# Kernel tuning notes

Hardware: AMD Instinct MI355X
Metric: run time of the kernel (lower is better)

Reference implementation:

```python
import jax, jax.numpy as jnp
import numpy as np

# Fixed production-scale sizes (equal-sized graphs so unbatch == reshape)
B, NQ, ND = 64, 32, 512     # graph pairs, query nodes/graph, data nodes/graph
DIN, D, K = 64, 128, 16     # GCN_in_size, GCN_out_size, NTN_k
DEG = 8                     # average degree


def _gcn(x, src, dst, W, b):
    """GCNConv with self loops + symmetric normalization (PyG semantics)."""
    N = x.shape[0]
    loop = jnp.arange(N)
    s = jnp.concatenate([src, loop])
    t = jnp.concatenate([dst, loop])
    deg = jax.ops.segment_sum(jnp.ones_like(t, x.dtype), t, num_segments=N)
    dinv = jnp.where(deg > 0, deg ** -0.5, 0.0)
    norm = (dinv[s] * dinv[t])[:, None]
    h = x @ W
    return jax.ops.segment_sum(h[s] * norm, t, num_segments=N) + b


def _three_gcn(x, ei, W1, b1, W2, b2, W3, b3):
    src, dst = ei[0], ei[1]
    h1 = jax.nn.relu(_gcn(x, src, dst, W1, b1))
    h2 = jax.nn.relu(_gcn(h1, src, dst, W2, b2))
    h3 = jax.nn.relu(_gcn(h2, src, dst, W3, b3))
    return h1, h2, h3


def _level(q, d, Wn, Vn, bn, cw, cb):
    """att_layer + NTN + elementwise mult + 1x1 conv + softmax over data nodes.
    q: [B,NQ,D], d: [B,ND,D] -> (softmaxed map [B,NQ,ND], raw map, he [B,K,NQ,ND])."""
    att = jax.nn.softmax(jnp.einsum('bqd,bnd->bqn', q, d) / jnp.sqrt(jnp.float32(D)), axis=-1)
    qW = jnp.einsum('bqd,kde->bkqe', q, Wn)           # [B,K,NQ,D]
    bil = jnp.einsum('bkqe,bne->bkqn', qW, d)          # [B,K,NQ,ND]
    lq = jnp.einsum('kd,bqd->bkq', Vn[:, :D], q)[:, :, :, None]
    ld = jnp.einsum('kd,bnd->bkn', Vn[:, D:], d)[:, :, None, :]
    he = jax.nn.sigmoid(bil + lq + ld + bn[None, :, None, None]) * att[:, None]
    e_raw = jnp.einsum('k,bkqn->bqn', cw, he) + cb     # 1x1 Conv2d(K->1)
    return jax.nn.softmax(e_raw, axis=-1), e_raw, he


def reference(x_d, edge_index_d, x_q, edge_index_q, batch_index_d, batch_index_q,
              W1, b1, W2, b2, W3, b3,
              Wn1, Vn1, bn1, cw1, cb1,
              Wn2, Vn2, bn2, cw2, cb2,
              Wn3, Vn3, bn3, cw3, cb3,
              w_end, b_end):
    d1, d2, d3 = _three_gcn(x_d, edge_index_d, W1, b1, W2, b2, W3, b3)
    q1, q2, q3 = _three_gcn(x_q, edge_index_q, W1, b1, W2, b2, W3, b3)
    # unbatch: batch indices are sorted with equal graph sizes -> reshape
    d1, d2, d3 = (t.reshape(B, ND, D) for t in (d1, d2, d3))
    q1, q2, q3 = (t.reshape(B, NQ, D) for t in (q1, q2, q3))
    e1, _, he1 = _level(q1, d1, Wn1, Vn1, bn1, cw1, cb1)
    _, e2raw, he2 = _level(q2, d2, Wn2, Vn2, bn2, cw2, cb2)
    e3, _, he3 = _level(q3, d3, Wn3, Vn3, bn3, cw3, cb3)
    # Faithful to source quirks: the zip unpack `e1,e2,e3,h1,h2,h1` rebinds h1 to
    # he_3 (he_1 is never used, he_3 appears twice) and end2 enters the concat
    # PRE-softmax (the softmaxed version was assigned to unused `nd2`).
    stack = jnp.concatenate([e1[:, None], e2raw[:, None], e3[:, None], he3, he2, he3], axis=1)
    out = jnp.einsum('c,bcqn->bqn', w_end, stack) + b_end  # con_end 1x1 conv + squeeze
    return jax.nn.softmax(out, axis=-1)                    # softmax over data nodes


def setup_inputs() -> dict:
    key = jax.random.key(0)
    k = jax.random.split(key, 40)
    n = jax.random.normal
    Nd, Nq = B * ND, B * NQ
    Ed, Eq = Nd * DEG, Nq * DEG
    gid_d = jnp.repeat(jnp.arange(B), ND * DEG)
    gid_q = jnp.repeat(jnp.arange(B), NQ * DEG)
    inp = {
        'x_d': n(k[0], (Nd, DIN), jnp.float32),
        'x_q': n(k[1], (Nq, DIN), jnp.float32),
        'edge_index_d': jnp.stack([jax.random.randint(k[2], (Ed,), 0, ND) + gid_d * ND,
                                   jax.random.randint(k[3], (Ed,), 0, ND) + gid_d * ND]),
        'edge_index_q': jnp.stack([jax.random.randint(k[4], (Eq,), 0, NQ) + gid_q * NQ,
                                   jax.random.randint(k[5], (Eq,), 0, NQ) + gid_q * NQ]),
        'batch_index_d': jnp.repeat(jnp.arange(B), ND),
        'batch_index_q': jnp.repeat(jnp.arange(B), NQ),
        'W1': n(k[6], (DIN, D), jnp.float32) / np.sqrt(DIN), 'b1': jnp.zeros((D,), jnp.float32),
        'W2': n(k[7], (D, D), jnp.float32) / np.sqrt(D), 'b2': jnp.zeros((D,), jnp.float32),
        'W3': n(k[8], (D, D), jnp.float32) / np.sqrt(D), 'b3': jnp.zeros((D,), jnp.float32),
    }
    for i, l in enumerate(('1', '2', '3')):
        inp['Wn' + l] = n(k[10 + 4 * i], (K, D, D), jnp.float32) / np.sqrt(D)
        inp['Vn' + l] = n(k[11 + 4 * i], (K, 2 * D), jnp.float32) / np.sqrt(2 * D)
        inp['bn' + l] = jnp.zeros((K,), jnp.float32)
        inp['cw' + l] = n(k[12 + 4 * i], (K,), jnp.float32) / np.sqrt(K)
        inp['cb' + l] = jnp.zeros((1,), jnp.float32)
    inp['w_end'] = n(k[25], (3 * K + 3,), jnp.float32) / np.sqrt(3 * K + 3)
    inp['b_end'] = jnp.zeros((1,), jnp.float32)
    return inp
```

## Files before the change

### kernel.cpp

```cpp
#include <hip/hip_runtime.h>
#include <math.h>

namespace {
constexpr int cB  = 64;
constexpr int cNQ = 32;
constexpr int cND = 512;
constexpr int cNd = cB * cND;
constexpr int cNq = cB * cNQ;
constexpr int cEd = cNd * 8;
constexpr int cEq = cNq * 8;
constexpr int LD_STRIDE = 516;
constexpr int NB_CSRD = 64;
constexpr int NB_CSRQ = 8;
constexpr int CVT0 = NB_CSRD + NB_CSRQ;
constexpr int NB_CVT = 2188;
constexpr int TR0 = CVT0 + NB_CVT;
constexpr int NB_T2BF = 808;
}

#define F4C(p) (*(const float4*)(p))

typedef __attribute__((ext_vector_type(8))) __bf16 bf16x8;
typedef __attribute__((ext_vector_type(4))) float floatx4;

__device__ __forceinline__ ushort f2bf(float f) {
  union { float f; unsigned u; } v;
  v.f = f;
  unsigned u = v.u;
  return (ushort)((u + 0x7fffu + ((u >> 16) & 1u)) >> 16);
}
__device__ __forceinline__ float bf2f(ushort u) {
  union { unsigned u; float f; } v;
  v.u = ((unsigned)u) << 16;
  return v.f;
}
__device__ __forceinline__ float4 us4f4(ushort4 u) {
  return make_float4(bf2f(u.x), bf2f(u.y), bf2f(u.z), bf2f(u.w));
}
__device__ __forceinline__ ushort4 f4us4(float4 f) {
  ushort4 o;
  o.x = f2bf(f.x); o.y = f2bf(f.y); o.z = f2bf(f.z); o.w = f2bf(f.w);
  return o;
}
__device__ __forceinline__ float fexp2(float x) {
#if __has_builtin(__builtin_amdgcn_exp2f)
  return __builtin_amdgcn_exp2f(x);
#else
  return exp2f(x);
#endif
}
__device__ __forceinline__ float frcp(float x) {
#if __has_builtin(__builtin_amdgcn_rcpf)
  return __builtin_amdgcn_rcpf(x);
#else
  return 1.0f / x;
#endif
}
__device__ __forceinline__ float fsigmoid(float z) {
  return frcp(1.0f + fexp2(z * -1.4426950408889634f));
}
__device__ __forceinline__ float fexp(float x) { return fexp2(x * 1.4426950408889634f); }

__device__ __forceinline__ int swz_g(int j) { return (((j >> 3) & 7) << 3) | (j & 7); }

__global__ __launch_bounds__(256) void k_front_csr(
    const float* __restrict__ xd, const float* __restrict__ xq,
    const float* __restrict__ v0, const float* __restrict__ v1,
    const float* __restrict__ v2, ushort* __restrict__ oxd, ushort* __restrict__ oxq,
    ushort* __restrict__ ov0, ushort* __restrict__ ov1, ushort* __restrict__ ov2,
    const float* __restrict__ W1, const float* __restrict__ W2,
    const float* __restrict__ W3, const float* __restrict__ Wn0,
    const float* __restrict__ Wn1, const float* __restrict__ Wn2,
    ushort* __restrict__ o1, ushort* __restrict__ o2, ushort* __restrict__ o3,
    ushort* __restrict__ on0, ushort* __restrict__ on1, ushort* __restrict__ on2,
    const int* __restrict__ src_d, const int* __restrict__ dst_d,
    const int* __restrict__ src_q, const int* __restrict__ dst_q,
    int* __restrict__ cnt_d, int* __restrict__ cnt_q,
    int* __restrict__ rp_d, int* __restrict__ rp_q,
    float* __restrict__ dinv_d, float* __restrict__ dinv_q,
    int* __restrict__ col_d, int* __restrict__ col_q) {
  __shared__ float tile[32][33];
  __shared__ int s_cnt[512];
  __shared__ int s_base[512];
  __shared__ int s_cur[512];
  int blk = blockIdx.x, tid = threadIdx.x;
  if (blk < NB_CSRD) {
    int g = blk;
    const int* dstg = dst_d + g * 4096;
    const int* srcg = src_d + g * 4096;
    int nbase = g * 512;
    s_cnt[tid] = 0; s_cnt[tid + 256] = 0;
    __syncthreads();
    for (int e = tid; e < 4096; e += 256) atomicAdd(&s_cnt[dstg[e] - nbase], 1);
    __syncthreads();
    int c0 = s_cnt[tid], c1 = s_cnt[tid + 256];
    s_base[tid] = c0; s_base[tid + 256] = c1;
    __syncthreads();
    for (int off = 1; off < 512; off <<= 1) {
      int a = (tid >= off) ? s_base[tid - off] : 0;
      int b = (tid + 256 >= off) ? s_base[tid + 256 - off] : 0;
      __syncthreads();
      s_base[tid] += a; s_base[tid + 256] += b;
      __syncthreads();
    }
    int e0 = s_base[tid] - c0, e1 = s_base[tid + 256] - c1;
    s_base[tid] = e0; s_base[tid + 256] = e1;
    s_cur[tid] = 0; s_cur[tid + 256] = 0;
    cnt_d[nbase + tid] = c0;
    cnt_d[nbase + tid + 256] = c1;
    rp_d[nbase + tid] = g * 4096 + e0;
    rp_d[nbase + tid + 256] = g * 4096 + e1;
    dinv_d[nbase + tid] = 1.0f / sqrtf((float)(c0 + 1));
    dinv_d[nbase + tid + 256] = 1.0f / sqrtf((float)(c1 + 1));
    __syncthreads();
    for (int e = tid; e < 4096; e += 256) {
      int d = dstg[e] - nbase;
      int p = atomicAdd(&s_cur[d], 1);
      col_d[g * 4096 + s_base[d] + p] = srcg[e];
    }
  } else if (blk < CVT0) {
    int qb = blk - NB_CSRD;
    int lg = tid >> 5, lane32 = tid & 31;
    int g = qb * 8 + lg;
    const int* dstg = dst_q + g * 256;
    const int* srcg = src_q + g * 256;
    int nbase = g * 32;
    s_cnt[tid] = 0;
    __syncthreads();
#pragma unroll
    for (int j = 0; j < 8; ++j)
      atomicAdd(&s_cnt[lg * 32 + (dstg[lane32 + j * 32] - nbase)], 1);
    __syncthreads();
    int v = s_cnt[tid];
    int incl = v;
#pragma unroll
    for (int off = 1; off < 32; off <<= 1) {
      int t = __shfl_up(incl, off, 32);
      if (lane32 >= off) incl += t;
    }
    int excl = incl - v;
    cnt_q[nbase + lane32] = v;
    rp_q[nbase + lane32] = g * 256 + excl;
    dinv_q[nbase + lane32] = 1.0f / sqrtf((float)(v + 1));
    s_base[tid] = excl;
    s_cur[tid] = 0;
    __syncthreads();
#pragma unroll
    for (int j = 0; j < 8; ++j) {
      int e = lane32 + j * 32;
      int d = dstg[e] - nbase;
      int p = atomicAdd(&s_cur[lg * 32 + d], 1);
      col_q[g * 256 + s_base[lg * 32 + d] + p] = srcg[e];
    }
  } else if (blk < TR0) {
    int b2 = blk - CVT0;
    const float* src;
    ushort* dst;
    int i;
    if (b2 < 2048) { src = xd; dst = oxd; i = b2 * 256 + tid; }
    else if (b2 < 2176) { src = xq; dst = oxq; i = (b2 - 2048) * 256 + tid; }
    else if (b2 < 2180) { src = v0; dst = ov0; i = (b2 - 2176) * 256 + tid; }
    else if (b2 < 2184) { src = v1; dst = ov1; i = (b2 - 2180) * 256 + tid; }
    else { src = v2; dst = ov2; i = (b2 - 2184) * 256 + tid; }
    *(ushort4*)(dst + (size_t)i * 4) = f4us4(F4C(src + (size_t)i * 4));
  } else {
    int b5 = blk - TR0;
    const float* in;
    ushort* out;
    int R, C, bt, t;
    if (b5 < 8)        { in = W1;  out = o1;  R = 64;  C = 128; bt = 0; t = b5; }
    else if (b5 < 24)  { in = W2;  out = o2;  R = 128; C = 128; bt = 0; t = b5 - 8; }
    else if (b5 < 40)  { in = W3;  out = o3;  R = 128; C = 128; bt = 0; t = b5 - 24; }
    else if (b5 < 296) { in = Wn0; out = on0; R = 128; C = 128; bt = (b5 - 40) >> 4;  t = (b5 - 40) & 15; }
    else if (b5 < 552) { in = Wn1; out = on1; R = 128; C = 128; bt = (b5 - 296) >> 4; t = (b5 - 296) & 15; }
    else               { in = Wn2; out = on2; R = 128; C = 128; bt = (b5 - 552) >> 4; t = (b5 - 552) & 15; }
    int tilesC = C >> 5;
    int tr = t / tilesC, tc = t - tr * tilesC;
    int tx = tid & 31, ty = tid >> 5;
    const float* ib = in + (size_t)bt * R * C;
    ushort* ob = out + (size_t)bt * R * C;
#pragma unroll
    for (int i = 0; i < 4; ++i)
      tile[ty + i * 8][tx] = ib[(tr * 32 + ty + i * 8) * C + tc * 32 + tx];
    __syncthreads();
#pragma unroll
    for (int i = 0; i < 4; ++i)
      ob[(size_t)(tc * 32 + ty + i * 8) * R + tr * 32 + tx] = f2bf(tile[tx][ty + i * 8]);
  }
}

__global__ __launch_bounds__(256) void k_gemm1(
    const ushort* __restrict__ xdbf, const ushort* __restrict__ xqbf,
    const ushort* __restrict__ w1T, const float* __restrict__ dinv_d,
    const float* __restrict__ dinv_q, ushort* __restrict__ htmp) {
  int blk2 = blockIdx.x, tid = threadIdx.x;
  int wave = tid >> 6, lane = tid & 63;
  int col = lane & 15, quad = lane >> 4;
  bool isQ = blk2 >= 512;
  int node0;
  if (isQ) node0 = (blk2 - 512) * 64;
  else node0 = swz_g(blk2) * 512 + (blk2 >> 6) * 64;
  int mloc = node0 + wave * 16;
  const ushort* X = isQ ? xqbf : xdbf;
  const float* dv = isQ ? dinv_q : dinv_d;
  size_t hbase = isQ ? (size_t)cNd : 0;
  floatx4 acc[8];
#pragma unroll
  for (int ct = 0; ct < 8; ++ct)
#pragma unroll
    for (int r = 0; r < 4; ++r) acc[ct][r] = 0.0f;
#pragma unroll
  for (int kc = 0; kc < 2; ++kc) {
    bf16x8 a = *(const bf16x8*)(X + (size_t)(mloc + col) * 64 + kc * 32 + quad * 8);
#pragma unroll
    for (int ct = 0; ct < 8; ++ct) {
      bf16x8 b = *(const bf16x8*)(w1T + (size_t)(ct * 16 + col) * 64 + kc * 32 + quad * 8);
      acc[ct] = __builtin_amdgcn_mfma_f32_16x16x32_bf16(a, b, acc[ct], 0, 0, 0);
    }
  }
  float sc[4];
#pragma unroll
  for (int r = 0; r < 4; ++r) sc[r] = dv[mloc + quad * 4 + r];
#pragma unroll
  for (int ct = 0; ct < 8; ++ct)
#pragma unroll
    for (int r = 0; r < 4; ++r)
      htmp[(hbase + mloc + quad * 4 + r) * 128 + ct * 16 + col] = f2bf(acc[ct][r] * sc[r]);
}

__global__ __launch_bounds__(256) void gmn_gather_merged(
    const ushort* __restrict__ htmp, const int* __restrict__ rp_d,
    const int* __restrict__ cnt_d, const int* __restrict__ col_d,
    const float* __restrict__ dinv_d, const int* __restrict__ rp_q,
    const int* __restrict__ cnt_q, const int* __restrict__ col_q,
    const float* __restrict__ dinv_q, const float* __restrict__ bias,
    ushort* __restrict__ dbf, ushort* __restrict__ qbf) {
  int blk = blockIdx.x, tid = threadIdx.x;
  bool isQ = blk >= 4096;
  int node;
  if (isQ) {
    int j = blk - 4096;
    node = swz_g(j) * 32 + (j >> 6) * 8 + (tid >> 5);
  } else {
    node = swz_g(blk) * 512 + (blk >> 6) * 8 + (tid >> 5);
  }
  int l = tid & 31;
  const ushort* hs = htmp + (isQ ? (size_t)cNd * 128 : 0);
  const int* rp = isQ ? rp_q : rp_d;
  const int* cnt = isQ ? cnt_q : cnt_d;
  const int* col = isQ ? col_q : col_d;
  const float* dinv = isQ ? dinv_q : dinv_d;
  ushort* outp = isQ ? qbf : dbf;
  int c = cnt[node], s0 = rp[node];
  float dt = dinv[node];
  float4 acc = us4f4(*(const ushort4*)(hs + (size_t)node * 128 + l * 4));
  int cm = c < 32 ? c : 32;
  for (int j0 = 0; j0 < cm; j0 += 8) {
    int ss[8];
    ushort4 v[8];
#pragma unroll
    for (int t = 0; t < 8; ++t) {
      int jj = j0 + t;
      ss[t] = (jj < cm) ? col[s0 + jj] : -1;
    }
#pragma unroll
    for (int t = 0; t < 8; ++t)
      if (ss[t] >= 0) v[t] = *(const ushort4*)(hs + (size_t)ss[t] * 128 + l * 4);
#pragma unroll
    for (int t = 0; t < 8; ++t) {
      if (ss[t] >= 0) {
        float4 f = us4f4(v[t]);
        acc.x += f.x; acc.y += f.y; acc.z += f.z; acc.w += f.w;
      }
    }
  }
  for (int j = 32; j < c; ++j) {
    int s = col[s0 + j];
    float4 f = us4f4(*(const ushort4*)(hs + (size_t)s * 128 + l * 4));
    acc.x += f.x; acc.y += f.y; acc.z += f.z; acc.w += f.w;
  }
  float4 bv = F4C(bias + l * 4);
  float4 r;
  r.x = fmaxf(acc.x * dt + bv.x, 0.0f);
  r.y = fmaxf(acc.y * dt + bv.y, 0.0f);
  r.z = fmaxf(acc.z * dt + bv.z, 0.0f);
  r.w = fmaxf(acc.w * dt + bv.w, 0.0f);
  *(ushort4*)(outp + (size_t)node * 128 + l * 4) = f4us4(r);
}

__global__ __launch_bounds__(512, 2) void k_level_gemm(
    const ushort* __restrict__ qbf, const ushort* __restrict__ dbf,
    const ushort* __restrict__ wnT, const ushort* __restrict__ vnbf,
    const float* __restrict__ bn, const float* __restrict__ cw,
    const float* __restrict__ w_end, const float* __restrict__ b_end,
    int o1, int o2, int hasF, int do_sm, int mode, int widx,
    float* __restrict__ accb, float* __restrict__ out,
    const ushort* __restrict__ gWT, const float* __restrict__ dinv_d,
    const float* __restrict__ dinv_q, ushort* __restrict__ htmp) {
  __shared__ float s_ld[16 * LD_STRIDE];
  __shared__ float s_lq[16 * 16];
  __shared__ float s_red[16 * 8];
  __shared__ __align__(16) ushort s_qw[4 * 16 * 128];
  int tid = threadIdx.x;
  int wave = tid >> 6, lane = tid & 63;
  int col = lane & 15, quad = lane >> 4;

  if (blockIdx.x >= 128) {
    int gblk = blockIdx.x - 128;
    bool isQ = gblk >= 256;
    int node0;
    if (isQ) node0 = (gblk - 256) * 128;
    else node0 = swz_g(gblk) * 512 + (gblk >> 6) * 128;
    int mloc = node0 + wave * 16;
    const ushort* X = isQ ? qbf : dbf;
    const float* dv = isQ ? dinv_q : dinv_d;
    size_t hbase = isQ ? (size_t)cNd : 0;
    floatx4 acc[8];
#pragma unroll
    for (int ct = 0; ct < 8; ++ct)
#pragma unroll
      for (int r = 0; r < 4; ++r) acc[ct][r] = 0.0f;
#pragma unroll
    for (int kc = 0; kc < 4; ++kc) {
      bf16x8 a = *(const bf16x8*)(X + (size_t)(mloc + col) * 128 + kc * 32 + quad * 8);
#pragma unroll
      for (int ct = 0; ct < 8; ++ct) {
        bf16x8 b = *(const bf16x8*)(gWT + (size_t)(ct * 16 + col) * 128 + kc * 32 + quad * 8);
        acc[ct] = __builtin_amdgcn_mfma_f32_16x16x32_bf16(a, b, acc[ct], 0, 0, 0);
      }
    }
    float sc[4];
#pragma unroll
    for (int r = 0; r < 4; ++r) sc[r] = dv[mloc + quad * 4 + r];
#pragma unroll
    for (int ct = 0; ct < 8; ++ct)
#pragma unroll
      for (int r = 0; r < 4; ++r)
        htmp[(hbase + mloc + quad * 4 + r) * 128 + ct * 16 + col] = f2bf(acc[ct][r] * sc[r]);
    return;
  }

  int b = swz_g(blockIdx.x & 63);
  int qh = blockIdx.x >> 6;
  int n0 = wave * 64;

  bf16x8 bfr[4][4];
#pragma unroll
  for (int s = 0; s < 4; ++s)
#pragma unroll
    for (int kc = 0; kc < 4; ++kc)
      bfr[s][kc] = *(const bf16x8*)(dbf + ((size_t)(b * 512 + n0 + s * 16 + col) << 7) +
                                    kc * 32 + quad * 8);
  bf16x8 aq[4];
#pragma unroll
  for (int kc = 0; kc < 4; ++kc)
    aq[kc] = *(const bf16x8*)(qbf + (size_t)(b * 32 + qh * 16 + col) * 128 +
                              kc * 32 + quad * 8);

  floatx4 att[4];
#pragma unroll
  for (int s = 0; s < 4; ++s)
#pragma unroll
    for (int r = 0; r < 4; ++r) att[s][r] = 0.0f;
#pragma unroll
  for (int kc = 0; kc < 4; ++kc)
#pragma unroll
    for (int s = 0; s < 4; ++s)
      att[s] = __builtin_amdgcn_mfma_f32_16x16x32_bf16(aq[kc], bfr[s][kc], att[s], 0, 0, 0);
  const float sc = 0.088388347648318440550f;
#pragma unroll
  for (int s = 0; s < 4; ++s)
#pragma unroll
    for (int r = 0; r < 4; ++r) att[s][r] *= sc;

  {
    bf16x8 vn2[4];
#pragma unroll
    for (int kc = 0; kc < 4; ++kc)
      vn2[kc] = *(const bf16x8*)(vnbf + col * 256 + 128 + kc * 32 + quad * 8);
#pragma unroll
    for (int s = 0; s < 4; ++s) {
      floatx4 lda;
#pragma unroll
      for (int r = 0; r < 4; ++r) lda[r] = 0.0f;
#pragma unroll
      for (int kc = 0; kc < 4; ++kc)
        lda = __builtin_amdgcn_mfma_f32_16x16x32_bf16(bfr[s][kc], vn2[kc], lda, 0, 0, 0);
#pragma unroll
      for (int r = 0; r < 4; ++r)
        s_ld[col * LD_STRIDE + n0 + s * 16 + quad * 4 + r] = lda[r];
    }
  }
  if (wave == 0) {
    bf16x8 vn1[4];
#pragma unroll
    for (int kc = 0; kc < 4; ++kc)
      vn1[kc] = *(const bf16x8*)(vnbf + col * 256 + kc * 32 + quad * 8);
    floatx4 lqa;
#pragma unroll
    for (int r = 0; r < 4; ++r) lqa[r] = 0.0f;
#pragma unroll
    for (int kc = 0; kc < 4; ++kc)
      lqa = __builtin_amdgcn_mfma_f32_16x16x32_bf16(aq[kc], vn1[kc], lqa, 0, 0, 0);
#pragma unroll
    for (int r = 0; r < 4; ++r) s_lq[col * 16 + quad * 4 + r] = lqa[r];
  }
  __syncthreads();

  float red[4], M[4];
#pragma unroll
  for (int r = 0; r < 4; ++r) {
    float m = fmaxf(fmaxf(att[0][r], att[1][r]), fmaxf(att[2][r], att[3][r]));
#pragma unroll
    for (int o = 1; o < 16; o <<= 1) m = fmaxf(m, __shfl_xor(m, o, 64));
    red[r] = m;
  }
  if (col == 0)
#pragma unroll
    for (int r = 0; r < 4; ++r) s_red[(quad * 4 + r) * 8 + wave] = red[r];
  __syncthreads();
#pragma unroll
  for (int r = 0; r < 4; ++r) {
    float m = s_red[(quad * 4 + r) * 8];
#pragma unroll
    for (int w = 1; w < 8; ++w) m = fmaxf(m, s_red[(quad * 4 + r) * 8 + w]);
    M[r] = m;
  }
  __syncthreads();
#pragma unroll
  for (int s = 0; s < 4; ++s)
#pragma unroll
    for (int r = 0; r < 4; ++r) att[s][r] = fexp(att[s][r] - M[r]);
#pragma unroll
  for (int r = 0; r < 4; ++r) {
    float m = att[0][r] + att[1][r] + att[2][r] + att[3][r];
#pragma unroll
    for (int o = 1; o < 16; o <<= 1) m += __shfl_xor(m, o, 64);
    red[r] = m;
  }
  if (col == 0)
#pragma unroll
    for (int r = 0; r < 4; ++r) s_red[(quad * 4 + r) * 8 + wave] = red[r];
  __syncthreads();
#pragma unroll
  for (int r = 0; r < 4; ++r) {
    float m = s_red[(quad * 4 + r) * 8];
#pragma unroll
    for (int w = 1; w < 8; ++w) m += s_red[(quad * 4 + r) * 8 + w];
    M[r] = frcp(m);
  }
  __syncthreads();
#pragma unroll
  for (int s = 0; s < 4; ++s)
#pragma unroll
    for (int r = 0; r < 4; ++r) att[s][r] *= M[r];

  floatx4 eacc[4], facc[4];
#pragma unroll
  for (int s = 0; s < 4; ++s)
#pragma unroll
    for (int r = 0; r < 4; ++r) { eacc[s][r] = 0.0f; facc[s][r] = 0.0f; }

  char* qws = (char*)s_qw;
  const int kk8 = wave >> 1;
  const int eh = wave & 1;
  for (int kb = 0; kb < 4; ++kb) {
    int kq = kb * 4 + kk8;
    __syncthreads();
#pragma unroll
    for (int ei = 0; ei < 4; ++ei) {
      floatx4 qa;
#pragma unroll
      for (int r = 0; r < 4; ++r) qa[r] = 0.0f;
#pragma unroll
      for (int kc = 0; kc < 4; ++kc) {
        bf16x8 bb = *(const bf16x8*)(wnT + (size_t)(kq * 128 + eh * 64 + ei * 16 + col) * 128 +
                                     kc * 32 + quad * 8);
        qa = __builtin_amdgcn_mfma_f32_16x16x32_bf16(aq[kc], bb, qa, 0, 0, 0);
      }
#pragma unroll
      for (int r = 0; r < 4; ++r) {
        int row = quad * 4 + r;
        int byte = (kk8 << 12) + row * 256 + (eh * 64 + ei * 16 + col) * 2;
        byte ^= (row & 7) << 4;
        *(ushort*)(qws + byte) = f2bf(qa[r]);
      }
    }
    __syncthreads();
#pragma unroll
    for (int kj = 0; kj < 4; ++kj) {
      int k = kb * 4 + kj;
      bf16x8 a0, a1, a2, a3;
      {
        int base = (kj << 12) + col * 256 + quad * 16;
        int swz = (col & 7) << 4;
        a0 = *(const bf16x8*)(qws + ((base) ^ swz));
        a1 = *(const bf16x8*)(qws + ((base + 64) ^ swz));
        a2 = *(const bf16x8*)(qws + ((base + 128) ^ swz));
        a3 = *(const bf16x8*)(qws + ((base + 192) ^ swz));
      }
      floatx4 bil[4];
#pragma unroll
      for (int s = 0; s < 4; ++s) {
#pragma unroll
        for (int r = 0; r < 4; ++r) bil[s][r] = 0.0f;
        bil[s] = __builtin_amdgcn_mfma_f32_16x16x32_bf16(a0, bfr[s][0], bil[s], 0, 0, 0);
        bil[s] = __builtin_amdgcn_mfma_f32_16x16x32_bf16(a1, bfr[s][1], bil[s], 0, 0, 0);
        bil[s] = __builtin_amdgcn_mfma_f32_16x16x32_bf16(a2, bfr[s][2], bil[s], 0, 0, 0);
        bil[s] = __builtin_amdgcn_mfma_f32_16x16x32_bf16(a3, bfr[s][3], bil[s], 0, 0, 0);
      }
      float bnk = bn[k], cwk = cw[k];
      float wkk = 0.0f;
      if (hasF) {
        wkk = w_end[o1 + k];
        if (o2 >= 0) wkk += w_end[o2 + k];
      }
      float lqv[4];
#pragma unroll
      for (int r = 0; r < 4; ++r) lqv[r] = s_lq[k * 16 + quad * 4 + r] + bnk;
#pragma unroll
      for (int s = 0; s < 4; ++s) {
        float ldv = s_ld[k * LD_STRIDE + n0 + s * 16 + col];
#pragma unroll
        for (int r = 0; r < 4; ++r) {
          float sg = fsigmoid(bil[s][r] + lqv[r] + ldv);
          eacc[s][r] += cwk * sg;
          facc[s][r] += wkk * sg;
        }
      }
    }
  }

#pragma unroll
  for (int s = 0; s < 4; ++s)
#pragma unroll
    for (int r = 0; r < 4; ++r) {
      eacc[s][r] *= att[s][r];
      facc[s][r] *= att[s][r];
    }
  if (do_sm) {
#pragma unroll
    for (int r = 0; r < 4; ++r) {
      float m = fmaxf(fmaxf(eacc[0][r], eacc[1][r]), fmaxf(eacc[2][r], eacc[3][r]));
#pragma unroll
      for (int o = 1; o < 16; o <<= 1) m = fmaxf(m, __shfl_xor(m, o, 64));
      red[r] = m;
    }
    if (col == 0)
#pragma unroll
      for (int r = 0; r < 4; ++r) s_red[(quad * 4 + r) * 8 + wave] = red[r];
    __syncthreads();
#pragma unroll
    for (int r = 0; r < 4; ++r) {
      float m = s_red[(quad * 4 + r) * 8];
#pragma unroll
      for (int w = 1; w < 8; ++w) m = fmaxf(m, s_red[(quad * 4 + r) * 8 + w]);
      M[r] = m;
    }
    __syncthreads();
#pragma unroll
    for (int s = 0; s < 4; ++s)
#pragma unroll
      for (int r = 0; r < 4; ++r) eacc[s][r] = fexp(eacc[s][r] - M[r]);
#pragma unroll
    for (int r = 0; r < 4; ++r) {
      float m = eacc[0][r] + eacc[1][r] + eacc[2][r] + eacc[3][r];
#pragma unroll
      for (int o = 1; o < 16; o <<= 1) m += __shfl_xor(m, o, 64);
      red[r] = m;
    }
    if (col == 0)
#pragma unroll
      for (int r = 0; r < 4; ++r) s_red[(quad * 4 + r) * 8 + wave] = red[r];
    __syncthreads();
#pragma unroll
    for (int r = 0; r < 4; ++r) {
      float m = s_red[(quad * 4 + r) * 8];
#pragma unroll
      for (int w = 1; w < 8; ++w) m += s_red[(quad * 4 + r) * 8 + w];
      M[r] = frcp(m);
    }
    __syncthreads();
#pragma unroll
    for (int s = 0; s < 4; ++s)
#pragma unroll
      for (int r = 0; r < 4; ++r) eacc[s][r] *= M[r];
  }
  float w = w_end[widx];
#pragma unroll
  for (int s = 0; s < 4; ++s)
#pragma unroll
    for (int r = 0; r < 4; ++r) eacc[s][r] = w * eacc[s][r] + (hasF ? facc[s][r] : 0.0f);

  if (mode == 0) {
#pragma unroll
    for (int s = 0; s < 4; ++s)
#pragma unroll
      for (int r = 0; r < 4; ++r)
        accb[((size_t)(b * 32 + qh * 16 + quad * 4 + r) << 9) + n0 + s * 16 + col] =
            eacc[s][r];
  } else if (mode == 1) {
#pragma unroll
    for (int s = 0; s < 4; ++s)
#pragma unroll
      for (int r = 0; r < 4; ++r)
        accb[((size_t)(b * 32 + qh * 16 + quad * 4 + r) << 9) + n0 + s * 16 + col] +=
            eacc[s][r];
  } else {
    float be = b_end[0];
#pragma unroll
    for (int s = 0; s < 4; ++s)
#pragma unroll
      for (int r = 0; r < 4; ++r)
        eacc[s][r] += accb[((size_t)(b * 32 + qh * 16 + quad * 4 + r) << 9) +
                           n0 + s * 16 + col] + be;
#pragma unroll
    for (int r = 0; r < 4; ++r) {
      float m = fmaxf(fmaxf(eacc[0][r], eacc[1][r]), fmaxf(eacc[2][r], eacc[3][r]));
#pragma unroll
      for (int o = 1; o < 16; o <<= 1) m = fmaxf(m, __shfl_xor(m, o, 64));
      red[r] = m;
    }
    if (col == 0)
#pragma unroll
      for (int r = 0; r < 4; ++r) s_red[(quad * 4 + r) * 8 + wave] = red[r];
    __syncthreads();
#pragma unroll
    for (int r = 0; r < 4; ++r) {
      float m = s_red[(quad * 4 + r) * 8];
#pragma unroll
      for (int w2 = 1; w2 < 8; ++w2) m = fmaxf(m, s_red[(quad * 4 + r) * 8 + w2]);
      M[r] = m;
    }
    __syncthreads();
#pragma unroll
    for (int s = 0; s < 4; ++s)
#pragma unroll
      for (int r = 0; r < 4; ++r) eacc[s][r] = fexp(eacc[s][r] - M[r]);
#pragma unroll
    for (int r = 0; r < 4; ++r) {
      float m = eacc[0][r] + eacc[1][r] + eacc[2][r] + eacc[3][r];
#pragma unroll
      for (int o = 1; o < 16; o <<= 1) m += __shfl_xor(m, o, 64);
      red[r] = m;
    }
    if (col == 0)
#pragma unroll
      for (int r = 0; r < 4; ++r) s_red[(quad * 4 + r) * 8 + wave] = red[r];
    __syncthreads();
#pragma unroll
    for (int r = 0; r < 4; ++r) {
      float m = s_red[(quad * 4 + r) * 8];
#pragma unroll
      for (int w2 = 1; w2 < 8; ++w2) m += s_red[(quad * 4 + r) * 8 + w2];
      M[r] = frcp(m);
    }
#pragma unroll
    for (int s = 0; s < 4; ++s)
#pragma unroll
      for (int r = 0; r < 4; ++r)
        out[((size_t)(b * 32 + qh * 16 + quad * 4 + r) << 9) + n0 + s * 16 + col] =
            eacc[s][r] * M[r];
  }
}

extern "C" void kernel_launch(void* const* d_in, const int* in_sizes, int n_in,
                              void* d_out, int out_size, void* d_ws, size_t ws_size,
                              hipStream_t stream) {
  (void)in_sizes; (void)n_in; (void)out_size; (void)ws_size;
  const float* x_d = (const float*)d_in[0];
  const float* x_q = (const float*)d_in[1];
  const int* ei_d = (const int*)d_in[2];
  const int* ei_q = (const int*)d_in[3];
  const float* W1 = (const float*)d_in[6];
  const float* b1 = (const float*)d_in[7];
  const float* W2 = (const float*)d_in[8];
  const float* b2 = (const float*)d_in[9];
  const float* W3 = (const float*)d_in[10];
  const float* b3 = (const float*)d_in[11];
  const float* Wn[3] = {(const float*)d_in[12], (const float*)d_in[17], (const float*)d_in[22]};
  const float* Vn[3] = {(const float*)d_in[13], (const float*)d_in[18], (const float*)d_in[23]};
  const float* bn[3] = {(const float*)d_in[14], (const float*)d_in[19], (const float*)d_in[24]};
  const float* cw[3] = {(const float*)d_in[15], (const float*)d_in[20], (const float*)d_in[25]};
  const float* w_end = (const float*)d_in[27];
  const float* b_end = (const float*)d_in[28];
  float* out = (float*)d_out;

  char* wsp = (char*)d_ws;
  auto alloc = [&](size_t nbytes) {
    void* p = (void*)wsp;
    wsp += (nbytes + 255) & ~(size_t)255;
    return p;
  };
  int* cnt_d = (int*)alloc(cNd * 4);
  int* cnt_q = (int*)alloc(cNq * 4);
  float* dinv_d = (float*)alloc(cNd * 4);
  float* dinv_q = (float*)alloc(cNq * 4);
  int* rp_d = (int*)alloc(cNd * 4);
  int* rp_q = (int*)alloc(cNq * 4);
  int* col_d = (int*)alloc((size_t)cEd * 4);
  int* col_q = (int*)alloc((size_t)cEq * 4);
  ushort* xdbf = (ushort*)alloc((size_t)cNd * 64 * 2);
  ushort* xqbf = (ushort*)alloc((size_t)cNq * 64 * 2);
  ushort* w1T = (ushort*)alloc(128 * 64 * 2);
  ushort* w2T = (ushort*)alloc(128 * 128 * 2);
  ushort* w3T = (ushort*)alloc(128 * 128 * 2);
  ushort* wnT[3];
  for (int l = 0; l < 3; ++l) wnT[l] = (ushort*)alloc((size_t)16 * 128 * 128 * 2);
  ushort* vnbf[3];
  for (int l = 0; l < 3; ++l) vnbf[l] = (ushort*)alloc(16 * 256 * 2);
  ushort* htmp = (ushort*)alloc((size_t)(cNd + cNq) * 128 * 2);
  ushort* dbf = (ushort*)alloc((size_t)cNd * 128 * 2);
  ushort* qbf[3];
  for (int l = 0; l < 3; ++l) qbf[l] = (ushort*)alloc((size_t)cNq * 128 * 2);
  float* accb = (float*)alloc((size_t)cB * cNQ * cND * 4);

  const int* src_d = ei_d;
  const int* dst_d = ei_d + cEd;
  const int* src_q = ei_q;
  const int* dst_q = ei_q + cEq;

  k_front_csr<<<TR0 + NB_T2BF, 256, 0, stream>>>(
      x_d, x_q, Vn[0], Vn[1], Vn[2], xdbf, xqbf, vnbf[0], vnbf[1], vnbf[2], W1, W2,
      W3, Wn[0], Wn[1], Wn[2], w1T, w2T, w3T, wnT[0], wnT[1], wnT[2],
      src_d, dst_d, src_q, dst_q, cnt_d, cnt_q, rp_d, rp_q, dinv_d, dinv_q,
      col_d, col_q);

  k_gemm1<<<544, 256, 0, stream>>>(xdbf, xqbf, w1T, dinv_d, dinv_q, htmp);

  const float* bias[3] = {b1, b2, b3};
  const ushort* nextWT[3] = {w2T, w3T, nullptr};
  const int o1s[3] = {0, 19, 3};
  const int o2s[3] = {-1, -1, 35};
  const int hasF[3] = {0, 1, 1};
  const int dosms[3] = {1, 0, 1};
  const int modes[3] = {0, 1, 2};

  for (int l = 0; l < 3; ++l) {
    gmn_gather_merged<<<(cNd + cNq) / 8, 256, 0, stream>>>(
        htmp, rp_d, cnt_d, col_d, dinv_d, rp_q, cnt_q, col_q, dinv_q, bias[l], dbf,
        qbf[l]);
    int grid = (l < 2) ? (128 + 272) : 128;
    k_level_gemm<<<grid, 512, 0, stream>>>(
        qbf[l], dbf, wnT[l], vnbf[l], bn[l], cw[l], w_end, b_end, o1s[l], o2s[l],
        hasF[l], dosms[l], modes[l], l, accb, out, nextWT[l], dinv_d, dinv_q, htmp);
  }
}
```

Measured before the change: 304.9 us.

## Use 1024-thread blocks and precompute all 16 NTN qW slices up front

The level kernel now runs 16 waves per block instead of 8. Each wave owns 32 data nodes instead of 64, and each wave computes one of the 16 K-slices of q·Wn into shared memory before the main loop. This removes the four-stage kb loop and its per-stage barriers, and the bilinear loop then reads all 16 slices from shared memory. The side GEMM blocks each cover 256 nodes, so fewer of them are launched. In exchange the kernel uses more LDS (a 64KB qW buffer), has fewer registers per thread, and drops the occupancy hint of two blocks per CU.

After: 311.8 us. +2.3%, slower.

```diff
diff --git a/kernel.cpp b/kernel.cpp
--- a/kernel.cpp
+++ b/kernel.cpp
@@ -16,6 +16,7 @@
 constexpr int NB_CVT = 2188;
 constexpr int TR0 = CVT0 + NB_CVT;
 constexpr int NB_T2BF = 808;
+constexpr int NB_GEMM2 = 136;
 }
 
 #define F4C(p) (*(const float4*)(p))
@@ -288,7 +289,7 @@
   *(ushort4*)(outp + (size_t)node * 128 + l * 4) = f4us4(r);
 }
 
-__global__ __launch_bounds__(512, 2) void k_level_gemm(
+__global__ __launch_bounds__(1024) void k_level_gemm(
     const ushort* __restrict__ qbf, const ushort* __restrict__ dbf,
     const ushort* __restrict__ wnT, const ushort* __restrict__ vnbf,
     const float* __restrict__ bn, const float* __restrict__ cw,
@@ -299,18 +300,18 @@
     const float* __restrict__ dinv_q, ushort* __restrict__ htmp) {
   __shared__ float s_ld[16 * LD_STRIDE];
   __shared__ float s_lq[16 * 16];
-  __shared__ float s_red[16 * 8];
-  __shared__ __align__(16) ushort s_qw[4 * 16 * 128];
+  __shared__ float s_red[16 * 16];
+  __shared__ __align__(16) ushort s_qw[16 * 16 * 128];
   int tid = threadIdx.x;
   int wave = tid >> 6, lane = tid & 63;
   int col = lane & 15, quad = lane >> 4;
 
   if (blockIdx.x >= 128) {
     int gblk = blockIdx.x - 128;
-    bool isQ = gblk >= 256;
+    bool isQ = gblk >= 128;
     int node0;
-    if (isQ) node0 = (gblk - 256) * 128;
-    else node0 = swz_g(gblk) * 512 + (gblk >> 6) * 128;
+    if (isQ) node0 = (gblk - 128) * 256;
+    else node0 = swz_g(gblk & 63) * 512 + (gblk >> 6) * 256;
     int mloc = node0 + wave * 16;
     const ushort* X = isQ ? qbf : dbf;
     const float* dv = isQ ? dinv_q : dinv_d;
@@ -342,11 +343,11 @@
 
   int b = swz_g(blockIdx.x & 63);
   int qh = blockIdx.x >> 6;
-  int n0 = wave * 64;
-
-  bf16x8 bfr[4][4];
-#pragma unroll
-  for (int s = 0; s < 4; ++s)
+  int n0 = wave * 32;
+
+  bf16x8 bfr[2][4];
+#pragma unroll
+  for (int s = 0; s < 2; ++s)
 #pragma unroll
     for (int kc = 0; kc < 4; ++kc)
       bfr[s][kc] = *(const bf16x8*)(dbf + ((size_t)(b * 512 + n0 + s * 16 + col) << 7) +
@@ -357,19 +358,43 @@
     aq[kc] = *(const bf16x8*)(qbf + (size_t)(b * 32 + qh * 16 + col) * 128 +
                               kc * 32 + quad * 8);
 
-  floatx4 att[4];
-#pragma unroll
-  for (int s = 0; s < 4; ++s)
+  {
+    char* qws = (char*)s_qw;
+    int kq = wave;
+#pragma unroll
+    for (int ei = 0; ei < 8; ++ei) {
+      floatx4 qa;
+#pragma unroll
+      for (int r = 0; r < 4; ++r) qa[r] = 0.0f;
+#pragma unroll
+      for (int kc = 0; kc < 4; ++kc) {
+        bf16x8 bb = *(const bf16x8*)(wnT + (size_t)(kq * 128 + ei * 16 + col) * 128 +
+                                     kc * 32 + quad * 8);
+        qa = __builtin_amdgcn_mfma_f32_16x16x32_bf16(aq[kc], bb, qa, 0, 0, 0);
+      }
+#pragma unroll
+      for (int r = 0; r < 4; ++r) {
+        int row = quad * 4 + r;
+        int byte = (kq << 12) + row * 256 + (ei * 16 + col) * 2;
+        byte ^= (row & 7) << 4;
+        *(ushort*)(qws + byte) = f2bf(qa[r]);
+      }
+    }
+  }
+
+  floatx4 att[2];
+#pragma unroll
+  for (int s = 0; s < 2; ++s)
 #pragma unroll
     for (int r = 0; r < 4; ++r) att[s][r] = 0.0f;
 #pragma unroll
   for (int kc = 0; kc < 4; ++kc)
 #pragma unroll
-    for (int s = 0; s < 4; ++s)
+    for (int s = 0; s < 2; ++s)
       att[s] = __builtin_amdgcn_mfma_f32_16x16x32_bf16(aq[kc], bfr[s][kc], att[s], 0, 0, 0);
   const float sc = 0.088388347648318440550f;
 #pragma unroll
-  for (int s = 0; s < 4; ++s)
+  for (int s = 0; s < 2; ++s)
 #pragma unroll
     for (int r = 0; r < 4; ++r) att[s][r] *= sc;
 
@@ -379,7 +404,7 @@
     for (int kc = 0; kc < 4; ++kc)
       vn2[kc] = *(const bf16x8*)(vnbf + col * 256 + 128 + kc * 32 + quad * 8);
 #pragma unroll
-    for (int s = 0; s < 4; ++s) {
+    for (int s = 0; s < 2; ++s) {
       floatx4 lda;
 #pragma unroll
       for (int r = 0; r < 4; ++r) lda[r] = 0.0f;
@@ -410,129 +435,102 @@
   float red[4], M[4];
 #pragma unroll
   for (int r = 0; r < 4; ++r) {
-    float m = fmaxf(fmaxf(att[0][r], att[1][r]), fmaxf(att[2][r], att[3][r]));
+    float m = fmaxf(att[0][r], att[1][r]);
 #pragma unroll
     for (int o = 1; o < 16; o <<= 1) m = fmaxf(m, __shfl_xor(m, o, 64));
     red[r] = m;
   }
   if (col == 0)
 #pragma unroll
-    for (int r = 0; r < 4; ++r) s_red[(quad * 4 + r) * 8 + wave] = red[r];
+    for (int r = 0; r < 4; ++r) s_red[(quad * 4 + r) * 16 + wave] = red[r];
   __syncthreads();
 #pragma unroll
   for (int r = 0; r < 4; ++r) {
-    float m = s_red[(quad * 4 + r) * 8];
-#pragma unroll
-    for (int w = 1; w < 8; ++w) m = fmaxf(m, s_red[(quad * 4 + r) * 8 + w]);
+    float m = s_red[(quad * 4 + r) * 16];
+#pragma unroll
+    for (int w = 1; w < 16; ++w) m = fmaxf(m, s_red[(quad * 4 + r) * 16 + w]);
     M[r] = m;
   }
   __syncthreads();
 #pragma unroll
-  for (int s = 0; s < 4; ++s)
+  for (int s = 0; s < 2; ++s)
 #pragma unroll
     for (int r = 0; r < 4; ++r) att[s][r] = fexp(att[s][r] - M[r]);
 #pragma unroll
   for (int r = 0; r < 4; ++r) {
-    float m = att[0][r] + att[1][r] + att[2][r] + att[3][r];
+    float m = att[0][r] + att[1][r];
 #pragma unroll
     for (int o = 1; o < 16; o <<= 1) m += __shfl_xor(m, o, 64);
     red[r] = m;
   }
   if (col == 0)
 #pragma unroll
-    for (int r = 0; r < 4; ++r) s_red[(quad * 4 + r) * 8 + wave] = red[r];
+    for (int r = 0; r < 4; ++r) s_red[(quad * 4 + r) * 16 + wave] = red[r];
   __syncthreads();
 #pragma unroll
   for (int r = 0; r < 4; ++r) {
-    float m = s_red[(quad * 4 + r) * 8];
-#pragma unroll
-    for (int w = 1; w < 8; ++w) m += s_red[(quad * 4 + r) * 8 + w];
+    float m = s_red[(quad * 4 + r) * 16];
+#pragma unroll
+    for (int w = 1; w < 16; ++w) m += s_red[(quad * 4 + r) * 16 + w];
     M[r] = frcp(m);
   }
   __syncthreads();
 #pragma unroll
-  for (int s = 0; s < 4; ++s)
+  for (int s = 0; s < 2; ++s)
 #pragma unroll
     for (int r = 0; r < 4; ++r) att[s][r] *= M[r];
 
-  floatx4 eacc[4], facc[4];
-#pragma unroll
-  for (int s = 0; s < 4; ++s)
+  floatx4 eacc[2], facc[2];
+#pragma unroll
+  for (int s = 0; s < 2; ++s)
 #pragma unroll
     for (int r = 0; r < 4; ++r) { eacc[s][r] = 0.0f; facc[s][r] = 0.0f; }
 
-  char* qws = (char*)s_qw;
-  const int kk8 = wave >> 1;
-  const int eh = wave & 1;
-  for (int kb = 0; kb < 4; ++kb) {
-    int kq = kb * 4 + kk8;
-    __syncthreads();
-#pragma unroll
-    for (int ei = 0; ei < 4; ++ei) {
-      floatx4 qa;
-#pragma unroll
-      for (int r = 0; r < 4; ++r) qa[r] = 0.0f;
-#pragma unroll
-      for (int kc = 0; kc < 4; ++kc) {
-        bf16x8 bb = *(const bf16x8*)(wnT + (size_t)(kq * 128 + eh * 64 + ei * 16 + col) * 128 +
-                                     kc * 32 + quad * 8);
-        qa = __builtin_amdgcn_mfma_f32_16x16x32_bf16(aq[kc], bb, qa, 0, 0, 0);
+  const char* qws = (const char*)s_qw;
+#pragma unroll 4
+  for (int k = 0; k < 16; ++k) {
+    bf16x8 a0, a1, a2, a3;
+    {
+      int base = (k << 12) + col * 256 + quad * 16;
+      int swz = (col & 7) << 4;
+      a0 = *(const bf16x8*)(qws + ((base) ^ swz));
+      a1 = *(const bf16x8*)(qws + ((base + 64) ^ swz));
+      a2 = *(const bf16x8*)(qws + ((base + 128) ^ swz));
+      a3 = *(const bf16x8*)(qws + ((base + 192) ^ swz));
+    }
+    floatx4 bil[2];
+#pragma unroll
+    for (int s = 0; s < 2; ++s) {
+#pragma unroll
+      for (int r = 0; r < 4; ++r) bil[s][r] = 0.0f;
+      bil[s] = __builtin_amdgcn_mfma_f32_16x16x32_bf16(a0, bfr[s][0], bil[s], 0, 0, 0);
+      bil[s] = __builtin_amdgcn_mfma_f32_16x16x32_bf16(a1, bfr[s][1], bil[s], 0, 0, 0);
+      bil[s] = __builtin_amdgcn_mfma_f32_16x16x32_bf16(a2, bfr[s][2], bil[s], 0, 0, 0);
+      bil[s] = __builtin_amdgcn_mfma_f32_16x16x32_bf16(a3, bfr[s][3], bil[s], 0, 0, 0);
+    }
+    float bnk = bn[k], cwk = cw[k];
+    float wkk = 0.0f;
+    if (hasF) {
+      wkk = w_end[o1 + k];
+      if (o2 >= 0) wkk += w_end[o2 + k];
+    }
+    float lqv[4];
+#pragma unroll
+    for (int r = 0; r < 4; ++r) lqv[r] = s_lq[k * 16 + quad * 4 + r] + bnk;
+#pragma unroll
+    for (int s = 0; s < 2; ++s) {
+      float ldv = s_ld[k * LD_STRIDE + n0 + s * 16 + col];
+#pragma unroll
+      for (int r = 0; r < 4; ++r) {
+        float sg = fsigmoid(bil[s][r] + lqv[r] + ldv);
+        eacc[s][r] += cwk * sg;
+        facc[s][r] += wkk * sg;
       }
-#pragma unroll
-      for (int r = 0; r < 4; ++r) {
-        int row = quad * 4 + r;
-        int byte = (kk8 << 12) + row * 256 + (eh * 64 + ei * 16 + col) * 2;
-        byte ^= (row & 7) << 4;
-        *(ushort*)(qws + byte) = f2bf(qa[r]);
-      }
-    }
-    __syncthreads();
-#pragma unroll
-    for (int kj = 0; kj < 4; ++kj) {
-      int k = kb * 4 + kj;
-      bf16x8 a0, a1, a2, a3;
-      {
-        int base = (kj << 12) + col * 256 + quad * 16;
-        int swz = (col & 7) << 4;
-        a0 = *(const bf16x8*)(qws + ((base) ^ swz));
-        a1 = *(const bf16x8*)(qws + ((base + 64) ^ swz));
-        a2 = *(const bf16x8*)(qws + ((base + 128) ^ swz));
-        a3 = *(const bf16x8*)(qws + ((base + 192) ^ swz));
-      }
-      floatx4 bil[4];
-#pragma unroll
-      for (int s = 0; s < 4; ++s) {
-#pragma unroll
-        for (int r = 0; r < 4; ++r) bil[s][r] = 0.0f;
-        bil[s] = __builtin_amdgcn_mfma_f32_16x16x32_bf16(a0, bfr[s][0], bil[s], 0, 0, 0);
-        bil[s] = __builtin_amdgcn_mfma_f32_16x16x32_bf16(a1, bfr[s][1], bil[s], 0, 0, 0);
-        bil[s] = __builtin_amdgcn_mfma_f32_16x16x32_bf16(a2, bfr[s][2], bil[s], 0, 0, 0);
-        bil[s] = __builtin_amdgcn_mfma_f32_16x16x32_bf16(a3, bfr[s][3], bil[s], 0, 0, 0);
-      }
-      float bnk = bn[k], cwk = cw[k];
-      float wkk = 0.0f;
-      if (hasF) {
-        wkk = w_end[o1 + k];
-        if (o2 >= 0) wkk += w_end[o2 + k];
-      }
-      float lqv[4];
-#pragma unroll
-      for (int r = 0; r < 4; ++r) lqv[r] = s_lq[k * 16 + quad * 4 + r] + bnk;
-#pragma unroll
-      for (int s = 0; s < 4; ++s) {
-        float ldv = s_ld[k * LD_STRIDE + n0 + s * 16 + col];
-#pragma unroll
-        for (int r = 0; r < 4; ++r) {
-          float sg = fsigmoid(bil[s][r] + lqv[r] + ldv);
-          eacc[s][r] += cwk * sg;
-          facc[s][r] += wkk * sg;
-        }
-      }
-    }
-  }
-
-#pragma unroll
-  for (int s = 0; s < 4; ++s)
+    }
+  }
+
+#pragma unroll
+  for (int s = 0; s < 2; ++s)
 #pragma unroll
     for (int r = 0; r < 4; ++r) {
       eacc[s][r] *= att[s][r];
@@ -541,67 +539,67 @@
   if (do_sm) {
 #pragma unroll
     for (int r = 0; r < 4; ++r) {
-      float m = fmaxf(fmaxf(eacc[0][r], eacc[1][r]), fmaxf(eacc[2][r], eacc[3][r]));
+      float m = fmaxf(eacc[0][r], eacc[1][r]);
 #pragma unroll
       for (int o = 1; o < 16; o <<= 1) m = fmaxf(m, __shfl_xor(m, o, 64));
       red[r] = m;
     }
     if (col == 0)
 #pragma unroll
-      for (int r = 0; r < 4; ++r) s_red[(quad * 4 + r) * 8 + wave] = red[r];
-    __syncthreads();
-#pragma unroll
-    for (int r = 0; r < 4; ++r) {
-      float m = s_red[(quad * 4 + r) * 8];
-#pragma unroll
-      for (int w = 1; w < 8; ++w) m = fmaxf(m, s_red[(quad * 4 + r) * 8 + w]);
+      for (int r = 0; r < 4; ++r) s_red[(quad * 4 + r) * 16 + wave] = red[r];
+    __syncthreads();
+#pragma unroll
+    for (int r = 0; r < 4; ++r) {
+      float m = s_red[(quad * 4 + r) * 16];
+#pragma unroll
+      for (int w = 1; w < 16; ++w) m = fmaxf(m, s_red[(quad * 4 + r) * 16 + w]);
       M[r] = m;
     }
     __syncthreads();
 #pragma unroll
-    for (int s = 0; s < 4; ++s)
+    for (int s = 0; s < 2; ++s)
 #pragma unroll
       for (int r = 0; r < 4; ++r) eacc[s][r] = fexp(eacc[s][r] - M[r]);
 #pragma unroll
     for (int r = 0; r < 4; ++r) {
-      float m = eacc[0][r] + eacc[1][r] + eacc[2][r] + eacc[3][r];
+      float m = eacc[0][r] + eacc[1][r];
 #pragma unroll
       for (int o = 1; o < 16; o <<= 1) m += __shfl_xor(m, o, 64);
       red[r] = m;
     }
     if (col == 0)
 #pragma unroll
-      for (int r = 0; r < 4; ++r) s_red[(quad * 4 + r) * 8 + wave] = red[r];
-    __syncthreads();
-#pragma unroll
-    for (int r = 0; r < 4; ++r) {
-      float m = s_red[(quad * 4 + r) * 8];
-#pragma unroll
-      for (int w = 1; w < 8; ++w) m += s_red[(quad * 4 + r) * 8 + w];
+      for (int r = 0; r < 4; ++r) s_red[(quad * 4 + r) * 16 + wave] = red[r];
+    __syncthreads();
+#pragma unroll
+    for (int r = 0; r < 4; ++r) {
+      float m = s_red[(quad * 4 + r) * 16];
+#pragma unroll
+      for (int w = 1; w < 16; ++w) m += s_red[(quad * 4 + r) * 16 + w];
       M[r] = frcp(m);
     }
     __syncthreads();
 #pragma unroll
-    for (int s = 0; s < 4; ++s)
+    for (int s = 0; s < 2; ++s)
 #pragma unroll
       for (int r = 0; r < 4; ++r) eacc[s][r] *= M[r];
   }
   float w = w_end[widx];
 #pragma unroll
-  for (int s = 0; s < 4; ++s)
+  for (int s = 0; s < 2; ++s)
 #pragma unroll
     for (int r = 0; r < 4; ++r) eacc[s][r] = w * eacc[s][r] + (hasF ? facc[s][r] : 0.0f);
 
   if (mode == 0) {
 #pragma unroll
-    for (int s = 0; s < 4; ++s)
+    for (int s = 0; s < 2; ++s)
 #pragma unroll
       for (int r = 0; r < 4; ++r)
         accb[((size_t)(b * 32 + qh * 16 + quad * 4 + r) << 9) + n0 + s * 16 + col] =
             eacc[s][r];
   } else if (mode == 1) {
 #pragma unroll
-    for (int s = 0; s < 4; ++s)
+    for (int s = 0; s < 2; ++s)
 #pragma unroll
       for (int r = 0; r < 4; ++r)
         accb[((size_t)(b * 32 + qh * 16 + quad * 4 + r) << 9) + n0 + s * 16 + col] +=
@@ -609,54 +607,54 @@
   } else {
     float be = b_end[0];
 #pragma unroll
-    for (int s = 0; s < 4; ++s)
+    for (int s = 0; s < 2; ++s)
 #pragma unroll
       for (int r = 0; r < 4; ++r)
         eacc[s][r] += accb[((size_t)(b * 32 + qh * 16 + quad * 4 + r) << 9) +
                            n0 + s * 16 + col] + be;
 #pragma unroll
     for (int r = 0; r < 4; ++r) {
-      float m = fmaxf(fmaxf(eacc[0][r], eacc[1][r]), fmaxf(eacc[2][r], eacc[3][r]));
+      float m = fmaxf(eacc[0][r], eacc[1][r]);
 #pragma unroll
       for (int o = 1; o < 16; o <<= 1) m = fmaxf(m, __shfl_xor(m, o, 64));
       red[r] = m;
     }
     if (col == 0)
 #pragma unroll
-      for (int r = 0; r < 4; ++r) s_red[(quad * 4 + r) * 8 + wave] = red[r];
-    __syncthreads();
-#pragma unroll
-    for (int r = 0; r < 4; ++r) {
-      float m = s_red[(quad * 4 + r) * 8];
-#pragma unroll
-      for (int w2 = 1; w2 < 8; ++w2) m = fmaxf(m, s_red[(quad * 4 + r) * 8 + w2]);
+      for (int r = 0; r < 4; ++r) s_red[(quad * 4 + r) * 16 + wave] = red[r];
+    __syncthreads();
+#pragma unroll
+    for (int r = 0; r < 4; ++r) {
+      float m = s_red[(quad * 4 + r) * 16];
+#pragma unroll
+      for (int w2 = 1; w2 < 16; ++w2) m = fmaxf(m, s_red[(quad * 4 + r) * 16 + w2]);
       M[r] = m;
     }
     __syncthreads();
 #pragma unroll
-    for (int s = 0; s < 4; ++s)
+    for (int s = 0; s < 2; ++s)
 #pragma unroll
       for (int r = 0; r < 4; ++r) eacc[s][r] = fexp(eacc[s][r] - M[r]);
 #pragma unroll
     for (int r = 0; r < 4; ++r) {
-      float m = eacc[0][r] + eacc[1][r] + eacc[2][r] + eacc[3][r];
+      float m = eacc[0][r] + eacc[1][r];
 #pragma unroll
       for (int o = 1; o < 16; o <<= 1) m += __shfl_xor(m, o, 64);
       red[r] = m;
     }
     if (col == 0)
 #pragma unroll
-      for (int r = 0; r < 4; ++r) s_red[(quad * 4 + r) * 8 + wave] = red[r];
-    __syncthreads();
-#pragma unroll
-    for (int r = 0; r < 4; ++r) {
-      float m = s_red[(quad * 4 + r) * 8];
-#pragma unroll
-      for (int w2 = 1; w2 < 8; ++w2) m += s_red[(quad * 4 + r) * 8 + w2];
+      for (int r = 0; r < 4; ++r) s_red[(quad * 4 + r) * 16 + wave] = red[r];
+    __syncthreads();
+#pragma unroll
+    for (int r = 0; r < 4; ++r) {
+      float m = s_red[(quad * 4 + r) * 16];
+#pragma unroll
+      for (int w2 = 1; w2 < 16; ++w2) m += s_red[(quad * 4 + r) * 16 + w2];
       M[r] = frcp(m);
     }
 #pragma unroll
-    for (int s = 0; s < 4; ++s)
+    for (int s = 0; s < 2; ++s)
 #pragma unroll
       for (int r = 0; r < 4; ++r)
         out[((size_t)(b * 32 + qh * 16 + quad * 4 + r) << 9) + n0 + s * 16 + col] =
@@ -740,8 +738,8 @@
     gmn_gather_merged<<<(cNd + cNq) / 8, 256, 0, stream>>>(
         htmp, rp_d, cnt_d, col_d, dinv_d, rp_q, cnt_q, col_q, dinv_q, bias[l], dbf,
         qbf[l]);
-    int grid = (l < 2) ? (128 + 272) : 128;
-    k_level_gemm<<<grid, 512, 0, stream>>>(
+    int grid = (l < 2) ? (128 + NB_GEMM2) : 128;
+    k_level_gemm<<<grid, 1024, 0, stream>>>(
         qbf[l], dbf, wnT[l], vnbf[l], bn[l], cw[l], w_end, b_end, o1s[l], o2s[l],
         hasF[l], dosms[l], modes[l], l, accb, out, nextWT[l], dinv_d, dinv_q, htmp);
   }
```
